# Kernel optimization log

Measured on AMD Instinct MI355X. Metric: run time of the kernel, lower is better.

## Reference

```python
import jax, jax.numpy as jnp
import numpy as np

B, F, D = 8192, 1024, 128  # batch, agent input feats, latent (Bernoulli) size


def setup_inputs() -> dict:
    key = jax.random.key(0)
    kx, kw = jax.random.split(key)
    x = jax.random.normal(kx, (B, F), dtype=jnp.float32)
    # scale so logits land in a non-degenerate range around [0,1]
    W = jax.random.normal(kw, (F, D), dtype=jnp.float32) * (1.0 / np.sqrt(F))
    b = jnp.zeros((D,), dtype=jnp.float32)
    return {"x": x, "W": W, "b": b}


def reference(x, W, b):
    """SparseMAPWrapper.forward with a linear agent, budget=0 (bernoulli_smap).

    SparseMAP over independent Bernoullis: mu* = clip(theta, 0, 1); the sparse
    distribution over bit-vector configurations is the nested-threshold
    decomposition of mu* (support <= D+1), padded with zero-weight rows.
    """
    theta = x @ W + b                      # [B, D] logits from the agent
    mu = jnp.clip(theta, 0.0, 1.0)         # SparseMAP marginals
    u = -jnp.sort(-mu, axis=-1)            # [B, D] descending
    # configs c_j = 1[mu >= u_j]; prepend the all-zeros configuration
    configs = (mu[:, None, :] >= u[:, :, None]).astype(theta.dtype)  # [B, D, D]
    zero_cfg = jnp.zeros((mu.shape[0], 1, mu.shape[1]), dtype=theta.dtype)
    sample = jnp.concatenate([zero_cfg, configs], axis=1)            # [B, D+1, D]
    # weights: w0 = 1 - u_1 (all-zeros), w_j = u_j - u_{j+1}, u_{D+1} = 0
    u_next = jnp.concatenate([u[:, 1:], jnp.zeros_like(u[:, :1])], axis=1)
    distr = jnp.concatenate([1.0 - u[:, :1], u - u_next], axis=1)    # [B, D+1]
    pos = distr > 0
    safe = jnp.where(pos, distr, 1.0)
    entropy_distr = jnp.sum(jnp.where(pos, -distr * jnp.log(safe), 0.0))
    entropy_distr = entropy_distr / distr.shape[0]
    support = jnp.sum(pos, axis=-1)        # [B] per-sample support sizes
    return sample, distr, entropy_distr, support
```

## Files before the change

### kernel.cpp

```cpp
#include <hip/hip_runtime.h>
#include <hip/hip_bf16.h>
#include <math.h>

#define BATCH 8192
#define FEAT  1024
#define DLAT  128
#define DP1   129

#define TILE_M 32
#define KT     32

__global__ __launch_bounds__(256) void gemm_theta(
    const float* __restrict__ x, const float* __restrict__ W,
    const float* __restrict__ b, float* __restrict__ theta) {
  __shared__ __align__(16) float xs[TILE_M][KT];
  __shared__ __align__(16) float wsh[KT][DLAT];
  const int row0 = blockIdx.x * TILE_M;
  const int t = threadIdx.x;
  const int c4 = (t & 31) * 4;
  const int r4 = (t >> 5) * 4;
  float acc[4][4] = {{0.f}};

  for (int k0 = 0; k0 < FEAT; k0 += KT) {
    {
      const int r  = t >> 3;
      const int cq = (t & 7) * 4;
      *(float4*)&xs[r][cq] =
          *(const float4*)(x + (size_t)(row0 + r) * FEAT + k0 + cq);
    }
    #pragma unroll
    for (int i = 0; i < 4; ++i) {
      const int idx = t + i * 256;
      const int kk  = idx >> 5;
      const int cq  = (idx & 31) * 4;
      *(float4*)&wsh[kk][cq] =
          *(const float4*)(W + (size_t)(k0 + kk) * DLAT + cq);
    }
    __syncthreads();
    #pragma unroll
    for (int kk = 0; kk < KT; ++kk) {
      float xv[4];
      #pragma unroll
      for (int r = 0; r < 4; ++r) xv[r] = xs[r4 + r][kk];
      const float4 w4 = *(const float4*)&wsh[kk][c4];
      const float wv[4] = {w4.x, w4.y, w4.z, w4.w};
      #pragma unroll
      for (int r = 0; r < 4; ++r)
        #pragma unroll
        for (int c = 0; c < 4; ++c)
          acc[r][c] = fmaf(xv[r], wv[c], acc[r][c]);
    }
    __syncthreads();
  }
  const float4 bv = *(const float4*)(b + c4);
  #pragma unroll
  for (int r = 0; r < 4; ++r) {
    float4 o;
    o.x = acc[r][0] + bv.x;
    o.y = acc[r][1] + bv.y;
    o.z = acc[r][2] + bv.z;
    o.w = acc[r][3] + bv.w;
    *(float4*)(theta + (size_t)(row0 + r4 + r) * DLAT + c4) = o;
  }
}

__global__ __launch_bounds__(256) void smap_rows(
    const float* __restrict__ theta, float* __restrict__ sample,
    float* __restrict__ distr, float* __restrict__ support,
    float* __restrict__ entpart) {
  __shared__ __align__(16) float mu[DLAT];
  __shared__ __align__(16) float s[DLAT];
  __shared__ float red[256];
  __shared__ int   redi[256];
  const int row = blockIdx.x;
  const int t = threadIdx.x;

  if (t < DLAT) {
    float v = theta[(size_t)row * DLAT + t];
    v = fminf(fmaxf(v, 0.0f), 1.0f);
    mu[t] = v;
    s[t]  = v;
  }
  __syncthreads();

  for (int k = 2; k <= DLAT; k <<= 1) {
    for (int j = k >> 1; j > 0; j >>= 1) {
      if (t < DLAT) {
        const int ixj = t ^ j;
        if (ixj > t) {
          const float a = s[t], bq = s[ixj];
          const bool up = ((t & k) == 0);
          const bool sw = up ? (a < bq) : (a > bq);
          if (sw) { s[t] = bq; s[ixj] = a; }
        }
      }
      __syncthreads();
    }
  }

  float w = 0.0f; int pos = 0; float ent = 0.0f;
  if (t < DP1) {
    if (t == 0)          w = 1.0f - s[0];
    else if (t < DLAT)   w = s[t - 1] - s[t];
    else                 w = s[DLAT - 1];
    distr[(size_t)row * DP1 + t] = w;
    if (w > 0.0f) { pos = 1; ent = -w * logf(w); }
  }
  red[t] = ent; redi[t] = pos;
  __syncthreads();
  for (int off = 128; off > 0; off >>= 1) {
    if (t < off) { red[t] += red[t + off]; redi[t] += redi[t + off]; }
    __syncthreads();
  }
  if (t == 0) {
    entpart[row] = red[0];
    support[row] = (float)redi[0];
  }

  const int jl = t >> 5;
  const int cq = (t & 31) * 4;
  float4* out = (float4*)(sample + (size_t)row * DP1 * DLAT);
  const float4 m4 = *(const float4*)&mu[cq];
  for (int jb = 0; jb < 136; jb += 8) {
    const int j = jb + jl;
    if (j < DP1) {
      const float thr = (j == 0) ? 2.0f : s[j - 1];
      float4 o;
      o.x = (m4.x >= thr) ? 1.0f : 0.0f;
      o.y = (m4.y >= thr) ? 1.0f : 0.0f;
      o.z = (m4.z >= thr) ? 1.0f : 0.0f;
      o.w = (m4.w >= thr) ? 1.0f : 0.0f;
      out[(size_t)j * (DLAT / 4) + (cq >> 2)] = o;
    }
  }
}

__global__ __launch_bounds__(256) void reduce_ent(
    const float* __restrict__ entpart, float* __restrict__ outent) {
  __shared__ double red[256];
  const int t = threadIdx.x;
  double acc = 0.0;
  for (int i = t; i < BATCH; i += 256) acc += (double)entpart[i];
  red[t] = acc;
  __syncthreads();
  for (int off = 128; off > 0; off >>= 1) {
    if (t < off) red[t] += red[t + off];
    __syncthreads();
  }
  if (t == 0) *outent = (float)(red[0] / (double)BATCH);
}

extern "C" void kernel_launch(void* const* d_in, const int* in_sizes, int n_in,
                              void* d_out, int out_size, void* d_ws, size_t ws_size,
                              hipStream_t stream) {
  const float* x = (const float*)d_in[0];
  const float* W = (const float*)d_in[1];
  const float* b = (const float*)d_in[2];

  float* out = (float*)d_out;
  const size_t n_sample = (size_t)BATCH * DP1 * DLAT;
  const size_t n_distr  = (size_t)BATCH * DP1;
  float* sample  = out;
  float* distr   = out + n_sample;
  float* entropy = out + n_sample + n_distr;
  float* support = out + n_sample + n_distr + 1;

  float* theta   = (float*)d_ws;
  float* entpart = theta + (size_t)BATCH * DLAT;

  gemm_theta<<<BATCH / TILE_M, 256, 0, stream>>>(x, W, b, theta);
  smap_rows<<<BATCH, 256, 0, stream>>>(theta, sample, distr, support, entpart);
  reduce_ent<<<1, 256, 0, stream>>>(entpart, entropy);
}
```

Before: 627.5 us.

## Double-buffer GEMM tiles, replace bitonic sort with rank sort, nontemporal sample stores

The GEMM now double-buffers its x and W shared-memory tiles, prefetching the next k-slice into registers while computing on the current one, and reads x with vectorized float4 loads. The per-row bitonic sort, which needed many barriers, is replaced by a counting rank sort: each thread counts how many values are larger (index-tiebroken) and scatters its value directly. The sample writes are fully unrolled without bounds checks and use nontemporal stores to avoid polluting the cache with the large output. The entropy reduction uses 1024 threads. The main cost is the large sample write, so the compute changes may matter less than the store behaviour.

```diff
diff --git a/kernel.cpp b/kernel.cpp
--- a/kernel.cpp
+++ b/kernel.cpp
@@ -7,51 +7,90 @@
 #define DLAT  128
 #define DP1   129
 
+typedef float f32x4 __attribute__((ext_vector_type(4)));
+
 #define TILE_M 32
 #define KT     32
+#define NK0    (FEAT / KT)
 
 __global__ __launch_bounds__(256) void gemm_theta(
     const float* __restrict__ x, const float* __restrict__ W,
     const float* __restrict__ b, float* __restrict__ theta) {
-  __shared__ __align__(16) float xs[TILE_M][KT];
-  __shared__ __align__(16) float wsh[KT][DLAT];
+  __shared__ __align__(16) float xs[2][TILE_M][KT];
+  __shared__ __align__(16) float wsh[2][KT][DLAT];
   const int row0 = blockIdx.x * TILE_M;
   const int t = threadIdx.x;
   const int c4 = (t & 31) * 4;
   const int r4 = (t >> 5) * 4;
+
+  const int lxr = t >> 3;
+  const int lxc = (t & 7) * 4;
   float acc[4][4] = {{0.f}};
 
-  for (int k0 = 0; k0 < FEAT; k0 += KT) {
-    {
-      const int r  = t >> 3;
-      const int cq = (t & 7) * 4;
-      *(float4*)&xs[r][cq] =
-          *(const float4*)(x + (size_t)(row0 + r) * FEAT + k0 + cq);
-    }
+  {
+    float4 px = *(const float4*)(x + (size_t)(row0 + lxr) * FEAT + lxc);
+    *(float4*)&xs[0][lxr][lxc] = px;
     #pragma unroll
     for (int i = 0; i < 4; ++i) {
       const int idx = t + i * 256;
       const int kk  = idx >> 5;
       const int cq  = (idx & 31) * 4;
-      *(float4*)&wsh[kk][cq] =
-          *(const float4*)(W + (size_t)(k0 + kk) * DLAT + cq);
+      *(float4*)&wsh[0][kk][cq] = *(const float4*)(W + (size_t)kk * DLAT + cq);
+    }
+  }
+  __syncthreads();
+
+  int buf = 0;
+  for (int k0it = 0; k0it < NK0; ++k0it) {
+    float4 px;
+    float4 pw[4];
+    const bool hasNext = (k0it + 1 < NK0);
+    if (hasNext) {
+      const int k0n = (k0it + 1) * KT;
+      px = *(const float4*)(x + (size_t)(row0 + lxr) * FEAT + k0n + lxc);
+      #pragma unroll
+      for (int i = 0; i < 4; ++i) {
+        const int idx = t + i * 256;
+        const int kk  = idx >> 5;
+        const int cq  = (idx & 31) * 4;
+        pw[i] = *(const float4*)(W + (size_t)(k0n + kk) * DLAT + cq);
+      }
+    }
+
+    #pragma unroll
+    for (int kk = 0; kk < KT; kk += 4) {
+      float4 xv[4], wv[4];
+      #pragma unroll
+      for (int r = 0; r < 4; ++r) xv[r] = *(const float4*)&xs[buf][r4 + r][kk];
+      #pragma unroll
+      for (int i = 0; i < 4; ++i) wv[i] = *(const float4*)&wsh[buf][kk + i][c4];
+      #pragma unroll
+      for (int r = 0; r < 4; ++r) {
+        const float* xr = (const float*)&xv[r];
+        #pragma unroll
+        for (int i = 0; i < 4; ++i) {
+          const float* wc = (const float*)&wv[i];
+          #pragma unroll
+          for (int c = 0; c < 4; ++c)
+            acc[r][c] = fmaf(xr[i], wc[c], acc[r][c]);
+        }
+      }
+    }
+
+    if (hasNext) {
+      *(float4*)&xs[buf ^ 1][lxr][lxc] = px;
+      #pragma unroll
+      for (int i = 0; i < 4; ++i) {
+        const int idx = t + i * 256;
+        const int kk  = idx >> 5;
+        const int cq  = (idx & 31) * 4;
+        *(float4*)&wsh[buf ^ 1][kk][cq] = pw[i];
+      }
     }
     __syncthreads();
-    #pragma unroll
-    for (int kk = 0; kk < KT; ++kk) {
-      float xv[4];
-      #pragma unroll
-      for (int r = 0; r < 4; ++r) xv[r] = xs[r4 + r][kk];
-      const float4 w4 = *(const float4*)&wsh[kk][c4];
-      const float wv[4] = {w4.x, w4.y, w4.z, w4.w};
-      #pragma unroll
-      for (int r = 0; r < 4; ++r)
-        #pragma unroll
-        for (int c = 0; c < 4; ++c)
-          acc[r][c] = fmaf(xv[r], wv[c], acc[r][c]);
-    }
-    __syncthreads();
-  }
+    buf ^= 1;
+  }
+
   const float4 bv = *(const float4*)(b + c4);
   #pragma unroll
   for (int r = 0; r < 4; ++r) {
@@ -79,24 +118,23 @@
     float v = theta[(size_t)row * DLAT + t];
     v = fminf(fmaxf(v, 0.0f), 1.0f);
     mu[t] = v;
-    s[t]  = v;
-  }
-  __syncthreads();
-
-  for (int k = 2; k <= DLAT; k <<= 1) {
-    for (int j = k >> 1; j > 0; j >>= 1) {
-      if (t < DLAT) {
-        const int ixj = t ^ j;
-        if (ixj > t) {
-          const float a = s[t], bq = s[ixj];
-          const bool up = ((t & k) == 0);
-          const bool sw = up ? (a < bq) : (a > bq);
-          if (sw) { s[t] = bq; s[ixj] = a; }
-        }
-      }
-      __syncthreads();
-    }
-  }
+  }
+  __syncthreads();
+
+  if (t < DLAT) {
+    const float v = mu[t];
+    int rank = 0;
+    #pragma unroll
+    for (int q = 0; q < DLAT / 4; ++q) {
+      const float4 m4 = *(const float4*)&mu[q * 4];
+      rank += (m4.x > v || (m4.x == v && (q * 4 + 0) < t)) ? 1 : 0;
+      rank += (m4.y > v || (m4.y == v && (q * 4 + 1) < t)) ? 1 : 0;
+      rank += (m4.z > v || (m4.z == v && (q * 4 + 2) < t)) ? 1 : 0;
+      rank += (m4.w > v || (m4.w == v && (q * 4 + 3) < t)) ? 1 : 0;
+    }
+    s[rank] = v;
+  }
+  __syncthreads();
 
   float w = 0.0f; int pos = 0; float ent = 0.0f;
   if (t < DP1) {
@@ -119,31 +157,39 @@
 
   const int jl = t >> 5;
   const int cq = (t & 31) * 4;
-  float4* out = (float4*)(sample + (size_t)row * DP1 * DLAT);
+  f32x4* out = (f32x4*)(sample + (size_t)row * DP1 * DLAT);
   const float4 m4 = *(const float4*)&mu[cq];
-  for (int jb = 0; jb < 136; jb += 8) {
-    const int j = jb + jl;
-    if (j < DP1) {
-      const float thr = (j == 0) ? 2.0f : s[j - 1];
-      float4 o;
-      o.x = (m4.x >= thr) ? 1.0f : 0.0f;
-      o.y = (m4.y >= thr) ? 1.0f : 0.0f;
-      o.z = (m4.z >= thr) ? 1.0f : 0.0f;
-      o.w = (m4.w >= thr) ? 1.0f : 0.0f;
-      out[(size_t)j * (DLAT / 4) + (cq >> 2)] = o;
-    }
-  }
-}
-
-__global__ __launch_bounds__(256) void reduce_ent(
+  #pragma unroll
+  for (int it = 0; it < 16; ++it) {
+    const int j = it * 8 + jl;
+    const float thr = (j == 0) ? 2.0f : s[j - 1];
+    f32x4 o;
+    o.x = (m4.x >= thr) ? 1.0f : 0.0f;
+    o.y = (m4.y >= thr) ? 1.0f : 0.0f;
+    o.z = (m4.z >= thr) ? 1.0f : 0.0f;
+    o.w = (m4.w >= thr) ? 1.0f : 0.0f;
+    __builtin_nontemporal_store(o, &out[(size_t)j * (DLAT / 4) + (cq >> 2)]);
+  }
+  if (jl == 0) {
+    const float thr = s[DLAT - 1];
+    f32x4 o;
+    o.x = (m4.x >= thr) ? 1.0f : 0.0f;
+    o.y = (m4.y >= thr) ? 1.0f : 0.0f;
+    o.z = (m4.z >= thr) ? 1.0f : 0.0f;
+    o.w = (m4.w >= thr) ? 1.0f : 0.0f;
+    __builtin_nontemporal_store(o, &out[(size_t)DLAT * (DLAT / 4) + (cq >> 2)]);
+  }
+}
+
+__global__ __launch_bounds__(1024) void reduce_ent(
     const float* __restrict__ entpart, float* __restrict__ outent) {
-  __shared__ double red[256];
+  __shared__ double red[1024];
   const int t = threadIdx.x;
   double acc = 0.0;
-  for (int i = t; i < BATCH; i += 256) acc += (double)entpart[i];
+  for (int i = t; i < BATCH; i += 1024) acc += (double)entpart[i];
   red[t] = acc;
   __syncthreads();
-  for (int off = 128; off > 0; off >>= 1) {
+  for (int off = 512; off > 0; off >>= 1) {
     if (t < off) red[t] += red[t + off];
     __syncthreads();
   }
@@ -170,5 +216,5 @@
 
   gemm_theta<<<BATCH / TILE_M, 256, 0, stream>>>(x, W, b, theta);
   smap_rows<<<BATCH, 256, 0, stream>>>(theta, sample, distr, support, entpart);
-  reduce_ent<<<1, 256, 0, stream>>>(entpart, entropy);
-}
+  reduce_ent<<<1, 1024, 0, stream>>>(entpart, entropy);
+}
```

New measurement: 622.3 us, median of 2. Within noise of the previous version (-0.8%).
